# Kernel optimization log

Hardware: AMD Instinct MI355X
Metric: run time of the kernel (lower is better)

Reference implementation:

```python
import jax, jax.numpy as jnp
import numpy as np
from jax import lax

KW, KH = 10, 20
D = KW * KH                # embed dim = 200
OC = 64                    # out channels = num_filt
FH = FW = 3                # filter size
NUM_ENT = 50000
NUM_REL = 474
B = 2048
FLAT = 2 * KW * KH * OC    # 25600
EPS = 1e-5


def chequer_perm(kw, kh):
    # faithful port of interleave_tensors_chessboard
    A = np.arange(kw * kh).reshape(kh, kw)
    Bm = np.arange(kw * kh, 2 * kw * kh).reshape(kh, kw)
    res = np.zeros((2 * kw, kh), dtype=np.int32)
    for i in range(kh):
        if i % 2 == 0:
            res[::2, i] = A[i]
            res[1::2, i] = Bm[i]
        else:
            res[::2, i] = Bm[i]
            res[1::2, i] = A[i]
    return res.T.reshape(-1)

PERM = jnp.asarray(chequer_perm(KW, KH))


def bn2d(x, g, b):
    # training-mode BatchNorm2d over (N,H,W), biased var
    m = x.mean((0, 2, 3), keepdims=True)
    v = x.var((0, 2, 3), keepdims=True)
    return g[None, :, None, None] * (x - m) / jnp.sqrt(v + EPS) + b[None, :, None, None]


def bn1d(x, g, b):
    m = x.mean(0, keepdims=True)
    v = x.var(0, keepdims=True)
    return g * (x - m) / jnp.sqrt(v + EPS) + b


def setup_inputs() -> dict:
    key = jax.random.key(0)
    ks = jax.random.split(key, 8)
    n_feats = jax.random.normal(ks[0], (NUM_ENT, D), dtype=jnp.float32) * 0.05
    r_feats = jax.random.normal(ks[1], (NUM_REL, D), dtype=jnp.float32) * 0.05
    # per-relation conv filters (padding_idx=0 -> zero row)
    filter_w = (jax.random.normal(ks[2], (NUM_REL, OC * FH * FW), dtype=jnp.float32) * 0.05).at[0].set(0.0)
    fc_w = jax.random.normal(ks[3], (D, FLAT), dtype=jnp.float32) * 0.01
    fc_b = jnp.zeros((D,), jnp.float32)
    bn0_g = jnp.ones((1,), jnp.float32); bn0_b = jnp.zeros((1,), jnp.float32)
    cbn_g = jnp.ones((OC,), jnp.float32); cbn_b = jnp.zeros((OC,), jnp.float32)
    bn1_g = jnp.ones((OC,), jnp.float32); bn1_b = jnp.zeros((OC,), jnp.float32)
    bn2_g = jnp.ones((D,), jnp.float32); bn2_b = jnp.zeros((D,), jnp.float32)
    ent_bias = jnp.zeros((NUM_ENT,), jnp.float32)
    sub = jax.random.randint(ks[4], (B,), 0, NUM_ENT)
    rel = jax.random.randint(ks[5], (B,), 0, NUM_REL)
    return dict(n_feats=n_feats, r_feats=r_feats, filter_w=filter_w,
                bn0_g=bn0_g, bn0_b=bn0_b, cbn_g=cbn_g, cbn_b=cbn_b,
                bn1_g=bn1_g, bn1_b=bn1_b, fc_w=fc_w, fc_b=fc_b,
                bn2_g=bn2_g, bn2_b=bn2_b, ent_bias=ent_bias, sub=sub, rel=rel)


def reference(n_feats, r_feats, filter_w, bn0_g, bn0_b, cbn_g, cbn_b,
              bn1_g, bn1_b, fc_w, fc_b, bn2_g, bn2_b, ent_bias, sub, rel):
    comb = jnp.concatenate([n_feats[sub], r_feats[rel]], axis=1)      # (B, 2D)
    x = comb[:, PERM].reshape(-1, 1, 2 * KW, KH)                      # (B,1,20,20)
    x = bn2d(x, bn0_g, bn0_b)
    bsz = x.shape[0]
    # per-sample dynamic filters via grouped conv (groups = batch)
    f = filter_w[rel].reshape(bsz * OC, 1, FH, FW)
    y = lax.conv_general_dilated(
        x.reshape(1, bsz, 2 * KW, KH), f,
        window_strides=(1, 1), padding=((FH // 2, FH // 2), (FW // 2, FW // 2)),
        feature_group_count=bsz, dimension_numbers=('NCHW', 'OIHW', 'NCHW'))
    y = y.reshape(bsz, OC, 2 * KW, KH)                                # (B,64,20,20)
    y = bn2d(y, cbn_g, cbn_b)   # Conv_with_Kernel.bn
    y = bn2d(y, bn1_g, bn1_b)   # outer bn1 (applied twice in original)
    y = jax.nn.relu(y)
    h = y.reshape(bsz, FLAT) @ fc_w.T + fc_b                          # (B, D)
    h = bn1d(h, bn2_g, bn2_b)
    h = jax.nn.relu(h)
    return h @ n_feats.T + ent_bias[None, :]                          # (B, NUM_ENT)
```

## Files before the change

kernel.cpp:

```cpp
#include <hip/hip_runtime.h>
#include <hip/hip_bf16.h>
#include <stddef.h>

typedef __attribute__((ext_vector_type(8))) short short8;
typedef __attribute__((ext_vector_type(4))) float f32x4;

#define EPSB 1e-5f
#define BSZ 2048
#define NENT 50000
#define KFC 25600
#define NPOP 819200.0f

__device__ __forceinline__ float bf2f(unsigned short h) {
    unsigned u = ((unsigned)h) << 16; float f; __builtin_memcpy(&f, &u, 4); return f;
}
__device__ __forceinline__ unsigned short f2bf(float f) {
    unsigned u; __builtin_memcpy(&u, &f, 4);
    unsigned r = u + 0x7fffu + ((u >> 16) & 1u);
    return (unsigned short)(r >> 16);
}

__global__ void k_gather(const float* __restrict__ nf, const float* __restrict__ rf,
                         const int* __restrict__ sub, const int* __restrict__ rel,
                         float* __restrict__ x, float* __restrict__ gpart) {
    int idx = blockIdx.x * 256 + threadIdx.x;
    int b = idx / 400, pos = idx % 400;
    int i = pos / 20, r = pos % 20;
    int src = i * 10 + (r >> 1) + (((i ^ r) & 1) * 200);
    float v = (src < 200) ? nf[(size_t)sub[b] * 200 + src]
                          : rf[(size_t)rel[b] * 200 + (src - 200)];
    x[idx] = v;
    float s1 = v, s2 = v * v;
    #pragma unroll
    for (int off = 32; off; off >>= 1) {
        s1 += __shfl_down(s1, off, 64);
        s2 += __shfl_down(s2, off, 64);
    }
    if ((threadIdx.x & 63) == 0) {
        int wid = blockIdx.x * 4 + (threadIdx.x >> 6);
        gpart[wid * 2]     = s1;
        gpart[wid * 2 + 1] = s2;
    }
}

__global__ void k_gfin(const float* __restrict__ gpart, float* __restrict__ stats) {
    int t = threadIdx.x;
    float s1 = 0.f, s2 = 0.f;
    for (int i = t; i < 12800; i += 256) {
        s1 += gpart[i * 2];
        s2 += gpart[i * 2 + 1];
    }
    #pragma unroll
    for (int off = 32; off; off >>= 1) {
        s1 += __shfl_down(s1, off, 64);
        s2 += __shfl_down(s2, off, 64);
    }
    __shared__ float red[8];
    if ((t & 63) == 0) { red[(t >> 6) * 2] = s1; red[(t >> 6) * 2 + 1] = s2; }
    __syncthreads();
    if (t == 0) {
        stats[0] = red[0] + red[2] + red[4] + red[6];
        stats[1] = red[1] + red[3] + red[5] + red[7];
    }
}

__global__ void k_fcw(const float* __restrict__ fcw, unsigned short* __restrict__ fcwb) {
    int idx = blockIdx.x * 256 + threadIdx.x;
    int d = idx / KFC, k = idx % KFC;
    float v = (d < 200) ? fcw[(size_t)d * KFC + k] : 0.f;
    fcwb[idx] = f2bf(v);
}

__global__ void k_nfb(const float* __restrict__ nf, unsigned short* __restrict__ nfb) {
    int idx = blockIdx.x * 256 + threadIdx.x;
    int e = idx / 224, k = idx % 224;
    float v = (e < NENT && k < 200) ? nf[(size_t)e * 200 + k] : 0.f;
    nfb[idx] = f2bf(v);
}

__global__ void k_conv(const float* __restrict__ x, const float* __restrict__ fw,
                       const int* __restrict__ rel,
                       const float* __restrict__ bn0g, const float* __restrict__ bn0b,
                       const float* __restrict__ stats,
                       unsigned short* __restrict__ z,
                       float* __restrict__ chpart) {
    __shared__ float xt[22 * 22];
    __shared__ float ft[576];
    __shared__ unsigned short zb[64 * 402];
    __shared__ float red[512];
    int b = blockIdx.x, t = threadIdx.x;

    float m0 = stats[0] * (1.f / NPOP);
    float v0 = fmaxf(stats[1] * (1.f / NPOP) - m0 * m0, 0.f);
    float inv0 = rsqrtf(v0 + EPSB);
    float a0 = bn0g[0] * inv0;
    float c0 = bn0b[0] - a0 * m0;

    for (int q = t; q < 484; q += 256) {
        int i = q / 22, j = q % 22;
        float val = 0.f;
        if (i >= 1 && i <= 20 && j >= 1 && j <= 20)
            val = a0 * x[b * 400 + (i - 1) * 20 + (j - 1)] + c0;
        xt[q] = val;
    }
    int rb = rel[b];
    for (int q = t; q < 576; q += 256) ft[q] = fw[(size_t)rb * 576 + q];
    __syncthreads();

    int oc = t >> 2, qq = t & 3;
    float f0 = ft[oc * 9 + 0], f1 = ft[oc * 9 + 1], f2 = ft[oc * 9 + 2];
    float f3 = ft[oc * 9 + 3], f4 = ft[oc * 9 + 4], f5 = ft[oc * 9 + 5];
    float f6 = ft[oc * 9 + 6], f7 = ft[oc * 9 + 7], f8 = ft[oc * 9 + 8];
    float cs1 = 0.f, cs2 = 0.f;
    #pragma unroll 4
    for (int p = 0; p < 100; ++p) {
        int pos = qq * 100 + p;
        int i = pos / 20, j = pos % 20;
        const float* xr = &xt[i * 22 + j];
        float acc = f0 * xr[0]  + f1 * xr[1]  + f2 * xr[2]
                  + f3 * xr[22] + f4 * xr[23] + f5 * xr[24]
                  + f6 * xr[44] + f7 * xr[45] + f8 * xr[46];
        zb[oc * 402 + pos] = f2bf(acc);
        cs1 += acc; cs2 += acc * acc;
    }
    red[t] = cs1; red[256 + t] = cs2;
    __syncthreads();
    if (t < 64) {
        float a  = red[t * 4] + red[t * 4 + 1] + red[t * 4 + 2] + red[t * 4 + 3];
        float sq = red[256 + t * 4] + red[256 + t * 4 + 1] + red[256 + t * 4 + 2] + red[256 + t * 4 + 3];
        chpart[(size_t)b * 128 + t]      = a;
        chpart[(size_t)b * 128 + 64 + t] = sq;
    }
    unsigned int* zout = (unsigned int*)(z + (size_t)b * KFC);
    #pragma unroll 2
    for (int kk = 0; kk < 50; ++kk) {
        int pidx = kk * 256 + t;
        int idx2 = pidx * 2;
        int o2 = idx2 / 400, p2 = idx2 % 400;
        zout[pidx] = *(const unsigned int*)&zb[o2 * 402 + p2];
    }
}

__global__ void k_chfin(const float* __restrict__ chpart,
                        const float* __restrict__ cg, const float* __restrict__ cb,
                        const float* __restrict__ g1, const float* __restrict__ b1,
                        float* __restrict__ scaleA, float* __restrict__ biasA) {
    int oc = blockIdx.x, t = threadIdx.x;
    float a = 0.f, sq = 0.f;
    for (int b = t; b < BSZ; b += 256) {
        a  += chpart[(size_t)b * 128 + oc];
        sq += chpart[(size_t)b * 128 + 64 + oc];
    }
    #pragma unroll
    for (int off = 32; off; off >>= 1) {
        a  += __shfl_down(a, off, 64);
        sq += __shfl_down(sq, off, 64);
    }
    __shared__ float red[8];
    if ((t & 63) == 0) { red[(t >> 6) * 2] = a; red[(t >> 6) * 2 + 1] = sq; }
    __syncthreads();
    if (t == 0) {
        float m = (red[0] + red[2] + red[4] + red[6]) * (1.f / NPOP);
        float v = fmaxf((red[1] + red[3] + red[5] + red[7]) * (1.f / NPOP) - m * m, 0.f);
        float d1 = v + EPSB;
        float varY = cg[oc] * cg[oc] * v / d1;
        float A = g1[oc] * cg[oc] * rsqrtf(d1) * rsqrtf(varY + EPSB);
        scaleA[oc] = A;
        biasA[oc]  = b1[oc] - A * m;
    }
}

__launch_bounds__(256)
__global__ void k_fc(const unsigned short* __restrict__ z, const unsigned short* __restrict__ fcwb,
                     const float* __restrict__ scaleA, const float* __restrict__ biasA,
                     float* __restrict__ hp) {
    __shared__ unsigned short Bt[208 * 40];
    int bx = blockIdx.x;
    int mblk = bx & 31, s = bx >> 5;
    int t = threadIdx.x, wave = t >> 6, lane = t & 63;
    int l15 = lane & 15, l4 = lane >> 4;

    f32x4 acc[13] = {};
    int row = mblk * 64 + wave * 16 + l15;
    const unsigned short* zrow = z + (size_t)row * KFC;
    int kbase0 = s * 1600;

    for (int st = 0; st < 50; ++st) {
        int kb = kbase0 + st * 32;
        __syncthreads();
        for (int idx = t; idx < 832; idx += 256) {
            int d = idx >> 2, g = idx & 3;
            *(uint4*)(&Bt[d * 40 + g * 8]) =
                *(const uint4*)(fcwb + (size_t)d * KFC + kb + g * 8);
        }
        __syncthreads();

        int k = kb + l4 * 8;
        uint4 araw = *(const uint4*)(zrow + k);
        int c = (unsigned)k / 400u;
        float Ac = scaleA[c], Bc = biasA[c];
        short8 af;
        const unsigned short* ap = (const unsigned short*)&araw;
        unsigned short* fp = (unsigned short*)&af;
        #pragma unroll
        for (int j = 0; j < 8; ++j) {
            float y = fmaxf(Ac * bf2f(ap[j]) + Bc, 0.f);
            fp[j] = f2bf(y);
        }
        #pragma unroll
        for (int nt = 0; nt < 13; ++nt) {
            short8 bf = *(const short8*)(&Bt[(nt * 16 + l15) * 40 + l4 * 8]);
            acc[nt] = __builtin_amdgcn_mfma_f32_16x16x32_bf16(af, bf, acc[nt], 0, 0, 0);
        }
    }
    float* hrow = hp + ((size_t)s * BSZ + (size_t)mblk * 64 + wave * 16) * 208;
    #pragma unroll
    for (int nt = 0; nt < 13; ++nt)
        #pragma unroll
        for (int r = 0; r < 4; ++r)
            hrow[(l4 * 4 + r) * 208 + nt * 16 + l15] = acc[nt][r];
}

__global__ void k_hred(const float* __restrict__ hp, float* __restrict__ h,
                       float* __restrict__ colsum, float* __restrict__ colsumsq) {
    int blk = blockIdx.x;
    int t = threadIdx.x;
    if (t >= 208) return;
    float cs = 0.f, css = 0.f;
    for (int r = 0; r < 64; ++r) {
        int row = blk * 64 + r;
        float v = 0.f;
        #pragma unroll
        for (int s2 = 0; s2 < 16; ++s2)
            v += hp[((size_t)s2 * BSZ + row) * 208 + t];
        h[(size_t)row * 208 + t] = v;
        cs += v; css += v * v;
    }
    atomicAdd(&colsum[t], cs); atomicAdd(&colsumsq[t], css);
}

__global__ void k_bnapply(const float* __restrict__ h,
                          const float* __restrict__ colsum, const float* __restrict__ colsumsq,
                          const float* __restrict__ g2, const float* __restrict__ b2,
                          unsigned short* __restrict__ h2) {
    int idx = blockIdx.x * 256 + threadIdx.x;
    int b = idx / 224, d = idx % 224;
    float out = 0.f;
    if (d < 200) {
        float m = colsum[d] * (1.f / 2048.f);
        float v = fmaxf(colsumsq[d] * (1.f / 2048.f) - m * m, 0.f);
        float val = g2[d] * (h[(size_t)b * 208 + d] - m) * rsqrtf(v + EPSB) + b2[d];
        out = fmaxf(val, 0.f);
    }
    h2[idx] = f2bf(out);
}

__launch_bounds__(256)
__global__ void k_out(const unsigned short* __restrict__ h2, const unsigned short* __restrict__ nfb,
                      const float* __restrict__ entb, float* __restrict__ out) {
    __shared__ unsigned short At[64 * 232];
    int bx = blockIdx.x;
    int mblk = bx & 31, nblk = bx >> 5;
    int t = threadIdx.x, wave = t >> 6, lane = t & 63;
    int l15 = lane & 15, l4 = lane >> 4;

    const unsigned short* hbase = h2 + (size_t)mblk * 64 * 224;
    for (int f = t; f < 1792; f += 256) {
        int row = f / 28, g = f % 28;
        *(uint4*)(&At[row * 232 + g * 8]) = *(const uint4*)(hbase + (size_t)row * 224 + g * 8);
    }
    __syncthreads();

    f32x4 acc[4] = {};
    int e = nblk * 64 + wave * 16 + l15;
    const unsigned short* brow = nfb + (size_t)e * 224;
    #pragma unroll
    for (int ks = 0; ks < 7; ++ks) {
        short8 bf = *(const short8*)(brow + ks * 32 + l4 * 8);
        #pragma unroll
        for (int mt = 0; mt < 4; ++mt) {
            short8 af = *(const short8*)(&At[(mt * 16 + l15) * 232 + ks * 32 + l4 * 8]);
            acc[mt] = __builtin_amdgcn_mfma_f32_16x16x32_bf16(af, bf, acc[mt], 0, 0, 0);
        }
    }
    if (e < NENT) {
        float eb = entb[e];
        #pragma unroll
        for (int mt = 0; mt < 4; ++mt) {
            #pragma unroll
            for (int r = 0; r < 4; ++r) {
                int row = mblk * 64 + mt * 16 + l4 * 4 + r;
                out[(size_t)row * NENT + e] = acc[mt][r] + eb;
            }
        }
    }
}

extern "C" void kernel_launch(void* const* d_in, const int* in_sizes, int n_in,
                              void* d_out, int out_size, void* d_ws, size_t ws_size,
                              hipStream_t stream) {
    const float* n_feats  = (const float*)d_in[0];
    const float* r_feats  = (const float*)d_in[1];
    const float* filter_w = (const float*)d_in[2];
    const float* bn0_g = (const float*)d_in[3];
    const float* bn0_b = (const float*)d_in[4];
    const float* cbn_g = (const float*)d_in[5];
    const float* cbn_b = (const float*)d_in[6];
    const float* bn1_g = (const float*)d_in[7];
    const float* bn1_b = (const float*)d_in[8];
    const float* fc_w  = (const float*)d_in[9];
    const float* bn2_g = (const float*)d_in[11];
    const float* bn2_b = (const float*)d_in[12];
    const float* ent_bias = (const float*)d_in[13];
    const int* sub = (const int*)d_in[14];
    const int* rel = (const int*)d_in[15];
    float* out = (float*)d_out;

    char* ws = (char*)d_ws;
    float*          stats = (float*)(ws + 0);
    float*          colsum  = stats + 130;
    float*          colsumsq= stats + 338;
    float*          scaleA  = stats + 1024;
    float*          biasA   = stats + 1088;
    float*          x    = (float*)(ws + 8192);
    unsigned short* z    = (unsigned short*)(ws + 3284992);
    unsigned short* fcwb = (unsigned short*)(ws + 108142592);
    float*          hp   = (float*)(ws + 118792192);
    float*          h    = (float*)(ws + 146055168);
    unsigned short* h2   = (unsigned short*)(ws + 147759104);
    unsigned short* nfb  = (unsigned short*)(ws + 148676608);

    float*          gpart  = (float*)(ws + 118792192);
    float*          chpart = (float*)(ws + 118792192 + 131072);

    hipMemsetAsync(stats, 0, 8192, stream);

    k_gather<<<3200, 256, 0, stream>>>(n_feats, r_feats, sub, rel, x, gpart);
    k_gfin<<<1, 256, 0, stream>>>(gpart, stats);
    k_fcw<<<20800, 256, 0, stream>>>(fc_w, fcwb);
    k_nfb<<<43792, 256, 0, stream>>>(n_feats, nfb);
    k_conv<<<2048, 256, 0, stream>>>(x, filter_w, rel, bn0_g, bn0_b, stats, z, chpart);
    k_chfin<<<64, 256, 0, stream>>>(chpart, cbn_g, cbn_b, bn1_g, bn1_b, scaleA, biasA);
    k_fc<<<512, 256, 0, stream>>>(z, fcwb, scaleA, biasA, hp);
    k_hred<<<32, 256, 0, stream>>>(hp, h, colsum, colsumsq);
    k_bnapply<<<1792, 256, 0, stream>>>(h, colsum, colsumsq, bn2_g, bn2_b, h2);
    k_out<<<25024, 256, 0, stream>>>(h2, nfb, ent_bias, out);
}
```

Baseline: 844.2 us.

## Vectorize casts, double-buffer FC GEMM, widen output tiles, unroll conv

The bf16 conversion kernels now handle eight elements per thread with float4 loads and 16-byte stores. The FC GEMM uses a double-buffered LDS tile with 64-wide K steps and register prefetch, so global loads overlap the MFMAs. The output GEMM tile grows to 128 rows, halving how often the entity-feature rows are reread, with B fragments preloaded. The conv loop is fully unrolled with paired outputs and packed stores, and the h reduction runs on more blocks. Costs include higher register and LDS use, which may lower occupancy.

Result: no change. 857.1 us (+1.5%).

```diff
diff --git a/kernel.cpp b/kernel.cpp
--- a/kernel.cpp
+++ b/kernel.cpp
@@ -66,16 +66,32 @@
 
 __global__ void k_fcw(const float* __restrict__ fcw, unsigned short* __restrict__ fcwb) {
     int idx = blockIdx.x * 256 + threadIdx.x;
-    int d = idx / KFC, k = idx % KFC;
-    float v = (d < 200) ? fcw[(size_t)d * KFC + k] : 0.f;
-    fcwb[idx] = f2bf(v);
+    int d = idx / 3200, g = idx % 3200;
+    int k = g * 8;
+    short8 o = {};
+    unsigned short* op = (unsigned short*)&o;
+    if (d < 200) {
+        float4 a = *(const float4*)(fcw + (size_t)d * KFC + k);
+        float4 b = *(const float4*)(fcw + (size_t)d * KFC + k + 4);
+        op[0] = f2bf(a.x); op[1] = f2bf(a.y); op[2] = f2bf(a.z); op[3] = f2bf(a.w);
+        op[4] = f2bf(b.x); op[5] = f2bf(b.y); op[6] = f2bf(b.z); op[7] = f2bf(b.w);
+    }
+    *(short8*)(fcwb + (size_t)idx * 8) = o;
 }
 
 __global__ void k_nfb(const float* __restrict__ nf, unsigned short* __restrict__ nfb) {
     int idx = blockIdx.x * 256 + threadIdx.x;
-    int e = idx / 224, k = idx % 224;
-    float v = (e < NENT && k < 200) ? nf[(size_t)e * 200 + k] : 0.f;
-    nfb[idx] = f2bf(v);
+    int e = idx / 28, g = idx % 28;
+    int k = g * 8;
+    short8 o = {};
+    unsigned short* op = (unsigned short*)&o;
+    if (e < NENT && k < 200) {
+        float4 a = *(const float4*)(nf + (size_t)e * 200 + k);
+        float4 b = *(const float4*)(nf + (size_t)e * 200 + k + 4);
+        op[0] = f2bf(a.x); op[1] = f2bf(a.y); op[2] = f2bf(a.z); op[3] = f2bf(a.w);
+        op[4] = f2bf(b.x); op[5] = f2bf(b.y); op[6] = f2bf(b.z); op[7] = f2bf(b.w);
+    }
+    *(short8*)(nfb + (size_t)idx * 8) = o;
 }
 
 __global__ void k_conv(const float* __restrict__ x, const float* __restrict__ fw,
@@ -112,16 +128,22 @@
     float f3 = ft[oc * 9 + 3], f4 = ft[oc * 9 + 4], f5 = ft[oc * 9 + 5];
     float f6 = ft[oc * 9 + 6], f7 = ft[oc * 9 + 7], f8 = ft[oc * 9 + 8];
     float cs1 = 0.f, cs2 = 0.f;
-    #pragma unroll 4
-    for (int p = 0; p < 100; ++p) {
-        int pos = qq * 100 + p;
-        int i = pos / 20, j = pos % 20;
-        const float* xr = &xt[i * 22 + j];
-        float acc = f0 * xr[0]  + f1 * xr[1]  + f2 * xr[2]
-                  + f3 * xr[22] + f4 * xr[23] + f5 * xr[24]
-                  + f6 * xr[44] + f7 * xr[45] + f8 * xr[46];
-        zb[oc * 402 + pos] = f2bf(acc);
-        cs1 += acc; cs2 += acc * acc;
+    #pragma unroll
+    for (int ri = 0; ri < 5; ++ri) {
+        int i = qq * 5 + ri;
+        const float* xr = &xt[i * 22];
+        #pragma unroll
+        for (int j = 0; j < 20; j += 2) {
+            float a0v = f0 * xr[j]      + f1 * xr[j + 1]  + f2 * xr[j + 2]
+                      + f3 * xr[j + 22] + f4 * xr[j + 23] + f5 * xr[j + 24]
+                      + f6 * xr[j + 44] + f7 * xr[j + 45] + f8 * xr[j + 46];
+            float a1v = f0 * xr[j + 1]  + f1 * xr[j + 2]  + f2 * xr[j + 3]
+                      + f3 * xr[j + 23] + f4 * xr[j + 24] + f5 * xr[j + 25]
+                      + f6 * xr[j + 45] + f7 * xr[j + 46] + f8 * xr[j + 47];
+            unsigned pk = (unsigned)f2bf(a0v) | ((unsigned)f2bf(a1v) << 16);
+            *(unsigned*)(&zb[oc * 402 + i * 20 + j]) = pk;
+            cs1 += a0v + a1v; cs2 += a0v * a0v + a1v * a1v;
+        }
     }
     red[t] = cs1; red[256 + t] = cs2;
     __syncthreads();
@@ -170,11 +192,23 @@
     }
 }
 
+__device__ __forceinline__ short8 cvt_affine(uint4 raw, float Ac, float Bc) {
+    short8 af;
+    const unsigned short* ap = (const unsigned short*)&raw;
+    unsigned short* fp = (unsigned short*)&af;
+    #pragma unroll
+    for (int j = 0; j < 8; ++j) {
+        float y = fmaxf(Ac * bf2f(ap[j]) + Bc, 0.f);
+        fp[j] = f2bf(y);
+    }
+    return af;
+}
+
 __launch_bounds__(256)
 __global__ void k_fc(const unsigned short* __restrict__ z, const unsigned short* __restrict__ fcwb,
                      const float* __restrict__ scaleA, const float* __restrict__ biasA,
                      float* __restrict__ hp) {
-    __shared__ unsigned short Bt[208 * 40];
+    __shared__ unsigned short Bt[2][208 * 72];
     int bx = blockIdx.x;
     int mblk = bx & 31, s = bx >> 5;
     int t = threadIdx.x, wave = t >> 6, lane = t & 63;
@@ -182,36 +216,64 @@
 
     f32x4 acc[13] = {};
     int row = mblk * 64 + wave * 16 + l15;
-    const unsigned short* zrow = z + (size_t)row * KFC;
-    int kbase0 = s * 1600;
-
-    for (int st = 0; st < 50; ++st) {
-        int kb = kbase0 + st * 32;
+    const unsigned short* zrow = z + (size_t)row * KFC + s * 1600;
+    const unsigned short* fbase = fcwb + s * 1600;
+
+    uint4 pre[7];
+    #pragma unroll
+    for (int j = 0; j < 7; ++j) {
+        int idx = t + j * 256;
+        if (idx < 1664) {
+            int d = idx >> 3, g = idx & 7;
+            pre[j] = *(const uint4*)(fbase + (size_t)d * KFC + g * 8);
+        }
+    }
+    uint4 zA = *(const uint4*)(zrow + l4 * 8);
+    uint4 zB = *(const uint4*)(zrow + 32 + l4 * 8);
+    #pragma unroll
+    for (int j = 0; j < 7; ++j) {
+        int idx = t + j * 256;
+        if (idx < 1664) { int d = idx >> 3, g = idx & 7; *(uint4*)(&Bt[0][d * 72 + g * 8]) = pre[j]; }
+    }
+    __syncthreads();
+
+    for (int st = 0; st < 25; ++st) {
+        int cur = st & 1;
+        uint4 zA2, zB2;
+        if (st + 1 < 25) {
+            #pragma unroll
+            for (int j = 0; j < 7; ++j) {
+                int idx = t + j * 256;
+                if (idx < 1664) {
+                    int d = idx >> 3, g = idx & 7;
+                    pre[j] = *(const uint4*)(fbase + (size_t)d * KFC + (st + 1) * 64 + g * 8);
+                }
+            }
+            zA2 = *(const uint4*)(zrow + (st + 1) * 64 + l4 * 8);
+            zB2 = *(const uint4*)(zrow + (st + 1) * 64 + 32 + l4 * 8);
+        }
+        int k0 = st * 64 + l4 * 8;
+        int kg0 = s * 1600 + k0;
+        int c0 = (unsigned)kg0 / 400u;
+        int c1 = (unsigned)(kg0 + 32) / 400u;
+        short8 af0 = cvt_affine(zA, scaleA[c0], biasA[c0]);
+        short8 af1 = cvt_affine(zB, scaleA[c1], biasA[c1]);
+        #pragma unroll
+        for (int nt = 0; nt < 13; ++nt) {
+            short8 bf0 = *(const short8*)(&Bt[cur][(nt * 16 + l15) * 72 + l4 * 8]);
+            acc[nt] = __builtin_amdgcn_mfma_f32_16x16x32_bf16(af0, bf0, acc[nt], 0, 0, 0);
+            short8 bf1 = *(const short8*)(&Bt[cur][(nt * 16 + l15) * 72 + 32 + l4 * 8]);
+            acc[nt] = __builtin_amdgcn_mfma_f32_16x16x32_bf16(af1, bf1, acc[nt], 0, 0, 0);
+        }
+        if (st + 1 < 25) {
+            #pragma unroll
+            for (int j = 0; j < 7; ++j) {
+                int idx = t + j * 256;
+                if (idx < 1664) { int d = idx >> 3, g = idx & 7; *(uint4*)(&Bt[cur ^ 1][d * 72 + g * 8]) = pre[j]; }
+            }
+            zA = zA2; zB = zB2;
+        }
         __syncthreads();
-        for (int idx = t; idx < 832; idx += 256) {
-            int d = idx >> 2, g = idx & 3;
-            *(uint4*)(&Bt[d * 40 + g * 8]) =
-                *(const uint4*)(fcwb + (size_t)d * KFC + kb + g * 8);
-        }
-        __syncthreads();
-
-        int k = kb + l4 * 8;
-        uint4 araw = *(const uint4*)(zrow + k);
-        int c = (unsigned)k / 400u;
-        float Ac = scaleA[c], Bc = biasA[c];
-        short8 af;
-        const unsigned short* ap = (const unsigned short*)&araw;
-        unsigned short* fp = (unsigned short*)&af;
-        #pragma unroll
-        for (int j = 0; j < 8; ++j) {
-            float y = fmaxf(Ac * bf2f(ap[j]) + Bc, 0.f);
-            fp[j] = f2bf(y);
-        }
-        #pragma unroll
-        for (int nt = 0; nt < 13; ++nt) {
-            short8 bf = *(const short8*)(&Bt[(nt * 16 + l15) * 40 + l4 * 8]);
-            acc[nt] = __builtin_amdgcn_mfma_f32_16x16x32_bf16(af, bf, acc[nt], 0, 0, 0);
-        }
     }
     float* hrow = hp + ((size_t)s * BSZ + (size_t)mblk * 64 + wave * 16) * 208;
     #pragma unroll
@@ -227,8 +289,8 @@
     int t = threadIdx.x;
     if (t >= 208) return;
     float cs = 0.f, css = 0.f;
-    for (int r = 0; r < 64; ++r) {
-        int row = blk * 64 + r;
+    for (int r = 0; r < 16; ++r) {
+        int row = blk * 16 + r;
         float v = 0.f;
         #pragma unroll
         for (int s2 = 0; s2 < 16; ++s2)
@@ -258,38 +320,41 @@
 __launch_bounds__(256)
 __global__ void k_out(const unsigned short* __restrict__ h2, const unsigned short* __restrict__ nfb,
                       const float* __restrict__ entb, float* __restrict__ out) {
-    __shared__ unsigned short At[64 * 232];
+    __shared__ unsigned short At[128 * 232];
     int bx = blockIdx.x;
-    int mblk = bx & 31, nblk = bx >> 5;
+    int mblk = bx & 15, nblk = bx >> 4;
     int t = threadIdx.x, wave = t >> 6, lane = t & 63;
     int l15 = lane & 15, l4 = lane >> 4;
 
-    const unsigned short* hbase = h2 + (size_t)mblk * 64 * 224;
-    for (int f = t; f < 1792; f += 256) {
+    const unsigned short* hbase = h2 + (size_t)mblk * 128 * 224;
+    for (int f = t; f < 3584; f += 256) {
         int row = f / 28, g = f % 28;
         *(uint4*)(&At[row * 232 + g * 8]) = *(const uint4*)(hbase + (size_t)row * 224 + g * 8);
     }
     __syncthreads();
 
-    f32x4 acc[4] = {};
+    f32x4 acc[8] = {};
     int e = nblk * 64 + wave * 16 + l15;
     const unsigned short* brow = nfb + (size_t)e * 224;
+    short8 bfr[7];
+    #pragma unroll
+    for (int ks = 0; ks < 7; ++ks)
+        bfr[ks] = *(const short8*)(brow + ks * 32 + l4 * 8);
     #pragma unroll
     for (int ks = 0; ks < 7; ++ks) {
-        short8 bf = *(const short8*)(brow + ks * 32 + l4 * 8);
-        #pragma unroll
-        for (int mt = 0; mt < 4; ++mt) {
+        #pragma unroll
+        for (int mt = 0; mt < 8; ++mt) {
             short8 af = *(const short8*)(&At[(mt * 16 + l15) * 232 + ks * 32 + l4 * 8]);
-            acc[mt] = __builtin_amdgcn_mfma_f32_16x16x32_bf16(af, bf, acc[mt], 0, 0, 0);
+            acc[mt] = __builtin_amdgcn_mfma_f32_16x16x32_bf16(af, bfr[ks], acc[mt], 0, 0, 0);
         }
     }
     if (e < NENT) {
         float eb = entb[e];
         #pragma unroll
-        for (int mt = 0; mt < 4; ++mt) {
+        for (int mt = 0; mt < 8; ++mt) {
             #pragma unroll
             for (int r = 0; r < 4; ++r) {
-                int row = mblk * 64 + mt * 16 + l4 * 4 + r;
+                int row = mblk * 128 + mt * 16 + l4 * 4 + r;
                 out[(size_t)row * NENT + e] = acc[mt][r] + eb;
             }
         }
@@ -337,12 +402,12 @@
 
     k_gather<<<3200, 256, 0, stream>>>(n_feats, r_feats, sub, rel, x, gpart);
     k_gfin<<<1, 256, 0, stream>>>(gpart, stats);
-    k_fcw<<<20800, 256, 0, stream>>>(fc_w, fcwb);
-    k_nfb<<<43792, 256, 0, stream>>>(n_feats, nfb);
+    k_fcw<<<2600, 256, 0, stream>>>(fc_w, fcwb);
+    k_nfb<<<5474, 256, 0, stream>>>(n_feats, nfb);
     k_conv<<<2048, 256, 0, stream>>>(x, filter_w, rel, bn0_g, bn0_b, stats, z, chpart);
     k_chfin<<<64, 256, 0, stream>>>(chpart, cbn_g, cbn_b, bn1_g, bn1_b, scaleA, biasA);
     k_fc<<<512, 256, 0, stream>>>(z, fcwb, scaleA, biasA, hp);
-    k_hred<<<32, 256, 0, stream>>>(hp, h, colsum, colsumsq);
+    k_hred<<<128, 256, 0, stream>>>(hp, h, colsum, colsumsq);
     k_bnapply<<<1792, 256, 0, stream>>>(h, colsum, colsumsq, bn2_g, bn2_b, h2);
-    k_out<<<25024, 256, 0, stream>>>(h2, nfb, ent_bias, out);
-}
+    k_out<<<12512, 256, 0, stream>>>(h2, nfb, ent_bias, out);
+}
```
